# Kernel tuning notes

Hardware: AMD Instinct MI355X
Metric: run time of the kernel (lower is better)

The kernel has to match this reference:

```python
import jax, jax.numpy as jnp
import numpy as np

NUM_CLASSES = 1000
FEATURE_DIM = 256
TEMPERATURE = 0.07
EPS = 1e-12  # matches torch F.normalize default eps


def setup_inputs() -> dict:
    key = jax.random.key(0)
    k1, k2, k3, k4 = jax.random.split(key, 4)
    N = 200000
    return {
        "src_feats": jax.random.normal(k1, (N, FEATURE_DIM), dtype=jnp.float32),
        "src_labels": jax.random.randint(k2, (N,), 0, NUM_CLASSES, dtype=jnp.int64),
        "tgt_feats": jax.random.normal(k3, (N, FEATURE_DIM), dtype=jnp.float32),
        "tgt_labels": jax.random.randint(k4, (N,), 0, NUM_CLASSES, dtype=jnp.int64),
    }


def _l2_normalize(x):
    norm = jnp.sqrt(jnp.sum(x * x, axis=1, keepdims=True))
    return x / jnp.maximum(norm, EPS)


def _prototype_init(features, labels):
    """Single-pass segment-mean replacing the per-class python loop.
    prototypes[c] = mean of features with label==c (0 if class absent)."""
    sums = jax.ops.segment_sum(features, labels, num_segments=NUM_CLASSES)  # [C, D]
    counts = jax.ops.segment_sum(jnp.ones_like(labels, dtype=features.dtype),
                                 labels, num_segments=NUM_CLASSES)          # [C]
    protos = sums / jnp.maximum(counts, 1.0)[:, None]
    return protos, counts


def _structure_matrix(protos):
    p = _l2_normalize(protos)
    return p @ p.T  # [C, C]


def reference(src_feats, src_labels, tgt_feats, tgt_labels):
    # PrototypeBank.update with detached features (first call: plain segment-mean)
    src_protos, _ = _prototype_init(jax.lax.stop_gradient(src_feats), src_labels)
    tgt_protos, _ = _prototype_init(jax.lax.stop_gradient(tgt_feats), tgt_labels)

    src_struct = _structure_matrix(src_protos)
    tgt_struct = _structure_matrix(tgt_protos)
    struct_loss = jnp.mean((src_struct - tgt_struct) ** 2)

    # contrastive loss: cosine logits against source prototypes, cross-entropy
    feats_n = _l2_normalize(src_feats)
    protos_n = _l2_normalize(src_protos)
    logits = (feats_n @ protos_n.T) / TEMPERATURE  # [N, C]
    logp = jax.nn.log_softmax(logits, axis=1)
    contrast_loss = -jnp.mean(jnp.take_along_axis(logp, src_labels[:, None], axis=1))

    return struct_loss, contrast_loss, src_protos, src_struct
```

## Files before the change

kernel.cpp:

```cpp
#include <hip/hip_runtime.h>
#include <hip/hip_fp8.h>

#define NCLS 1000
#define DIM 256
#define GCAP 500
#define NT16 64
#define SCLF 20.609930f
#define CP 23.0f
#define CPLN2 15.94238515f
#define LN2 0.69314718056f
#define PADC 2.86102294921875e-06f

typedef __attribute__((ext_vector_type(4))) float f32x4;
typedef long long i64;
typedef unsigned long long u64;

#if defined(__has_builtin) && __has_builtin(__builtin_amdgcn_cvt_pk_fp8_f32)
#define CVTPK(a, b, old, hi) __builtin_amdgcn_cvt_pk_fp8_f32((a), (b), (old), (hi))
#else
__device__ __forceinline__ unsigned cvtpk_sw(float a, float b, unsigned old, bool hi) {
  unsigned lo8 = __hip_cvt_float_to_fp8(a, __HIP_SATFINITE, __HIP_E4M3);
  unsigned hi8 = __hip_cvt_float_to_fp8(b, __HIP_SATFINITE, __HIP_E4M3);
  unsigned pk = lo8 | (hi8 << 8);
  return hi ? ((old & 0xffffu) | (pk << 16)) : ((old & 0xffff0000u) | pk);
}
#define CVTPK(a, b, old, hi) cvtpk_sw((a), (b), (old), (hi))
#endif

__device__ __forceinline__ float fexp2(float x) {
#if __has_builtin(__builtin_amdgcn_exp2f)
  return __builtin_amdgcn_exp2f(x);
#else
  return exp2f(x);
#endif
}

__global__ __launch_bounds__(256) void scatter_kernel(
    const int* __restrict__ sl, const int* __restrict__ tl, int N,
    int* __restrict__ gcnt, int* __restrict__ glist) {
  const int i = blockIdx.x * 256 + threadIdx.x;
  if (i >= 2 * N) return;
  const int side = (i >= N) ? 1 : 0;
  const int r = i - side * N;
  const int c = (side ? tl : sl)[r];
  const int bin = side * NCLS + c;
  const int slot = atomicAdd(gcnt + bin, 1);
  if (slot < GCAP) glist[(size_t)bin * GCAP + slot] = r;
}

__global__ __launch_bounds__(256) void proto_kernel(
    const float* __restrict__ sf, const float* __restrict__ tf,
    const int* __restrict__ gcnt, const int* __restrict__ glist,
    float* __restrict__ mean_out, float* __restrict__ spn, float* __restrict__ tpn,
    unsigned char* __restrict__ pbf8) {
  const int bid = blockIdx.x;
  const int side = (bid < NCLS) ? 1 : 0;
  const int c = side ? bid : (bid - NCLS);
  const int bin = side * NCLS + c;
  const float* feats = side ? tf : sf;
  const int* list = glist + (size_t)bin * GCAP;
  const int m = min(gcnt[bin], GCAP);
  const int t = threadIdx.x;
  __shared__ float s_red[4];

  float a0 = 0.f, a1 = 0.f, a2 = 0.f, a3 = 0.f, a4 = 0.f, a5 = 0.f, a6 = 0.f, a7 = 0.f;
  int i = 0;
  for (; i + 8 <= m; i += 8) {
    a0 += feats[(size_t)list[i + 0] * DIM + t];
    a1 += feats[(size_t)list[i + 1] * DIM + t];
    a2 += feats[(size_t)list[i + 2] * DIM + t];
    a3 += feats[(size_t)list[i + 3] * DIM + t];
    a4 += feats[(size_t)list[i + 4] * DIM + t];
    a5 += feats[(size_t)list[i + 5] * DIM + t];
    a6 += feats[(size_t)list[i + 6] * DIM + t];
    a7 += feats[(size_t)list[i + 7] * DIM + t];
  }
  for (; i < m; i++) a0 += feats[(size_t)list[i] * DIM + t];
  const float sum = ((a0 + a1) + (a2 + a3)) + ((a4 + a5) + (a6 + a7));
  const float mean = sum / fmaxf((float)m, 1.0f);
  if (!side) mean_out[(size_t)c * DIM + t] = mean;

  float ss = mean * mean;
  #pragma unroll
  for (int o = 1; o < 64; o <<= 1) ss += __shfl_xor(ss, o);
  if ((t & 63) == 0) s_red[t >> 6] = ss;
  __syncthreads();
  const float tot = s_red[0] + s_red[1] + s_red[2] + s_red[3];
  const float innv = 1.0f / fmaxf(sqrtf(tot), 1e-12f);
  const float p = mean * innv;
  (side ? tpn : spn)[(size_t)c * DIM + t] = p;
  if (!side) {
    size_t off = (size_t)(c >> 4) * 4096 + (size_t)(t >> 6) * 1024
               + (size_t)((t >> 3) & 3) * 256 + (size_t)(c & 15) * 16
               + (size_t)((t >> 5) & 1) * 8 + (t & 7);
    unsigned q = CVTPK(p, p, 0u, false);
    pbf8[off] = (unsigned char)(q & 0xffu);
  }
}

__global__ __launch_bounds__(256, 3) void fused_kernel(
    const float* __restrict__ feats, const int* __restrict__ labels,
    const unsigned char* __restrict__ pbf8, float* __restrict__ accp,
    const float* __restrict__ spn, const float* __restrict__ tpn,
    float* __restrict__ out_struct, float* __restrict__ acc,
    int N, int cblocks) {
  __shared__ __align__(16) unsigned char lds_raw[34816];
  const int bid = blockIdx.x;
  const int t = threadIdx.x;

  if (bid < 256) {
    float (*Sa)[68] = (float(*)[68])(lds_raw);
    float (*Sb)[68] = (float(*)[68])(lds_raw + 4352);
    float (*Ta)[68] = (float(*)[68])(lds_raw + 8704);
    float (*Tb)[68] = (float(*)[68])(lds_raw + 13056);
    float* red = (float*)(lds_raw + 17408);
    const int tx = t & 15, ty = t >> 4;
    const int i0 = (bid >> 4) * 64, j0 = (bid & 15) * 64;
    float cs[4][4], cg[4][4];
    #pragma unroll
    for (int a = 0; a < 4; a++)
      #pragma unroll
      for (int b = 0; b < 4; b++) { cs[a][b] = 0.f; cg[a][b] = 0.f; }

    const int srow = t >> 2;
    const int skq = (t & 3) * 4;
    for (int k0 = 0; k0 < DIM; k0 += 16) {
      __syncthreads();
      {
        float4 z = make_float4(0.f, 0.f, 0.f, 0.f);
        int ra = i0 + srow, rb = j0 + srow;
        float4 va = (ra < NCLS) ? *(const float4*)(spn + (size_t)ra * DIM + k0 + skq) : z;
        float4 vb = (rb < NCLS) ? *(const float4*)(spn + (size_t)rb * DIM + k0 + skq) : z;
        float4 wa = (ra < NCLS) ? *(const float4*)(tpn + (size_t)ra * DIM + k0 + skq) : z;
        float4 wb = (rb < NCLS) ? *(const float4*)(tpn + (size_t)rb * DIM + k0 + skq) : z;
        Sa[skq+0][srow]=va.x; Sa[skq+1][srow]=va.y; Sa[skq+2][srow]=va.z; Sa[skq+3][srow]=va.w;
        Sb[skq+0][srow]=vb.x; Sb[skq+1][srow]=vb.y; Sb[skq+2][srow]=vb.z; Sb[skq+3][srow]=vb.w;
        Ta[skq+0][srow]=wa.x; Ta[skq+1][srow]=wa.y; Ta[skq+2][srow]=wa.z; Ta[skq+3][srow]=wa.w;
        Tb[skq+0][srow]=wb.x; Tb[skq+1][srow]=wb.y; Tb[skq+2][srow]=wb.z; Tb[skq+3][srow]=wb.w;
      }
      __syncthreads();
      #pragma unroll
      for (int k = 0; k < 16; k++) {
        float a[4], b[4], c[4], d[4];
        *(float4*)a = *(const float4*)&Sa[k][ty * 4];
        *(float4*)b = *(const float4*)&Sb[k][tx * 4];
        *(float4*)c = *(const float4*)&Ta[k][ty * 4];
        *(float4*)d = *(const float4*)&Tb[k][tx * 4];
        #pragma unroll
        for (int ii = 0; ii < 4; ii++)
          #pragma unroll
          for (int jj = 0; jj < 4; jj++) {
            cs[ii][jj] = fmaf(a[ii], b[jj], cs[ii][jj]);
            cg[ii][jj] = fmaf(c[ii], d[jj], cg[ii][jj]);
          }
      }
    }
    float d2 = 0.f;
    #pragma unroll
    for (int ii = 0; ii < 4; ii++) {
      int gi = i0 + ty * 4 + ii;
      if (gi < NCLS) {
        #pragma unroll
        for (int jj = 0; jj < 4; jj++) {
          int gj = j0 + tx * 4 + jj;
          if (gj < NCLS) {
            out_struct[(size_t)gi * NCLS + gj] = cs[ii][jj];
            float df = cs[ii][jj] - cg[ii][jj];
            d2 += df * df;
          }
        }
      }
    }
    red[t] = d2;
    __syncthreads();
    for (int o = 128; o > 0; o >>= 1) { if (t < o) red[t] += red[t + o]; __syncthreads(); }
    if (t == 0) atomicAdd(acc, red[0]);
    return;
  }

  const int cbid = bid - 256;
  if (cbid >= cblocks) return;
  const int lane = t & 63;
  const int w = t >> 6;
  const int lx = lane & 15, lg = lane >> 4;
  const int row0 = cbid * 128 + w * 32;
  const float4 z4 = make_float4(0.f, 0.f, 0.f, 0.f);
  const unsigned char* bbase = pbf8 + (lg << 8) + (lx << 4);
  float* Aw = (float*)lds_raw + (size_t)w * (32 * 68);

  i64 af[2][8];
  float sclF[2][4];
  float sSt[2][4];
  int lbR[2];

  float n2a[2] = {0.f, 0.f};
  for (int kc = 0; kc < 4; kc++) {
    #pragma unroll
    for (int i = 0; i < 8; i++) {
      const int f = i * 64 + lane;
      const int row = f >> 4;
      const int c4 = f & 15;
      const int gr = row0 + row;
      float4 v = (gr < N) ? *(const float4*)(feats + (size_t)gr * DIM + kc * 64 + c4 * 4) : z4;
      *(float4*)&Aw[row * 68 + c4 * 4] = v;
    }
    #pragma unroll
    for (int rf = 0; rf < 2; rf++) {
      const int row = rf * 16 + lx;
      #pragma unroll
      for (int kk = 0; kk < 2; kk++) {
        float4 x = *(const float4*)&Aw[row * 68 + kk * 32 + lg * 8];
        float4 y = *(const float4*)&Aw[row * 68 + kk * 32 + lg * 8 + 4];
        n2a[rf] += x.x*x.x + x.y*x.y + x.z*x.z + x.w*x.w
                 + y.x*y.x + y.y*y.y + y.z*y.z + y.w*y.w;
        unsigned w0 = CVTPK(x.x, x.y, 0u, false);
        w0 = CVTPK(x.z, x.w, w0, true);
        unsigned w1 = CVTPK(y.x, y.y, 0u, false);
        w1 = CVTPK(y.z, y.w, w1, true);
        af[rf][kc * 2 + kk] = (i64)(((u64)w1 << 32) | (u64)w0);
      }
    }
  }
  #pragma unroll
  for (int rf = 0; rf < 2; rf++) {
    const int r = row0 + rf * 16 + lx;
    lbR[rf] = (r < N) ? labels[r] : 0;
    float n2 = n2a[rf];
    n2 += __shfl_xor(n2, 16);
    n2 += __shfl_xor(n2, 32);
    const float sw = SCLF / fmaxf(sqrtf(n2), 1e-12f);
    #pragma unroll
    for (int reg = 0; reg < 4; reg++) {
      sclF[rf][reg] = __shfl(sw, (lg << 2) | reg);
      sSt[rf][reg] = 0.f;
    }
  }

  int4 bA[4], bB[4];

  #define LOADB(dst_, cf_)                                                      \
    {                                                                           \
      const int4* gp = (const int4*)(bbase + ((size_t)(cf_) << 12));            \
      _Pragma("unroll")                                                         \
      for (int q = 0; q < 4; q++) dst_[q] = gp[q << 6];                         \
    }

  #define COMPUTE(buf_)                                                         \
    {                                                                           \
      f32x4 d0 = {0.f, 0.f, 0.f, 0.f};                                          \
      f32x4 d1 = {0.f, 0.f, 0.f, 0.f};                                          \
      _Pragma("unroll")                                                         \
      for (int q = 0; q < 4; q++) {                                             \
        i64 e0 = ((const i64*)&buf_[q])[0];                                     \
        i64 e1 = ((const i64*)&buf_[q])[1];                                     \
        d0 = __builtin_amdgcn_mfma_f32_16x16x32_fp8_fp8(af[0][2*q],   e0, d0, 0, 0, 0); \
        d1 = __builtin_amdgcn_mfma_f32_16x16x32_fp8_fp8(af[1][2*q],   e0, d1, 0, 0, 0); \
        d0 = __builtin_amdgcn_mfma_f32_16x16x32_fp8_fp8(af[0][2*q+1], e1, d0, 0, 0, 0); \
        d1 = __builtin_amdgcn_mfma_f32_16x16x32_fp8_fp8(af[1][2*q+1], e1, d1, 0, 0, 0); \
      }                                                                         \
      _Pragma("unroll")                                                         \
      for (int reg = 0; reg < 4; reg++) {                                       \
        sSt[0][reg] += fexp2(fmaf(d0[reg], sclF[0][reg], -CP));                 \
        sSt[1][reg] += fexp2(fmaf(d1[reg], sclF[1][reg], -CP));                 \
      }                                                                         \
    }

  LOADB(bA, 0);
  for (int cf = 0; cf < NT16; cf += 2) {
    LOADB(bB, cf + 1);
    COMPUTE(bA);
    if (cf + 2 < NT16) LOADB(bA, cf + 2);
    COMPUTE(bB);
  }

  float dvalS[2];
  #pragma unroll
  for (int rf = 0; rf < 2; rf++) {
    const int lb = lbR[rf];
    const unsigned char* gB = pbf8 + ((size_t)(lb >> 4) << 12) + (lg << 8)
                            + ((size_t)(lb & 15) << 4);
    f32x4 dL = {0.f, 0.f, 0.f, 0.f};
    #pragma unroll
    for (int q = 0; q < 4; q++) {
      int4 bg = *(const int4*)(gB + (q << 10));
      i64 e0 = ((const i64*)&bg)[0];
      i64 e1 = ((const i64*)&bg)[1];
      dL = __builtin_amdgcn_mfma_f32_16x16x32_fp8_fp8(af[rf][2*q],   e0, dL, 0, 0, 0);
      dL = __builtin_amdgcn_mfma_f32_16x16x32_fp8_fp8(af[rf][2*q+1], e1, dL, 0, 0, 0);
    }
    const int sel = lx & 3;
    dvalS[rf] = (sel == 0) ? dL[0] : (sel == 1) ? dL[1] : (sel == 2) ? dL[2] : dL[3];
  }

  float wl = 0.f;
  #pragma unroll
  for (int rf = 0; rf < 2; rf++)
    #pragma unroll
    for (int reg = 0; reg < 4; reg++) {
      float s = sSt[rf][reg];
      #pragma unroll
      for (int o = 1; o < 16; o <<= 1) s += __shfl_xor(s, o);
      const int j = (lg << 2) + reg;
      const float lbraw = __shfl(dvalS[rf], ((j >> 2) << 4) | j);
      const int row = row0 + rf * 16 + j;
      if (lx == 0 && row < N)
        wl += logf(s - PADC) + CPLN2 - lbraw * sclF[rf][reg] * LN2;
    }

  #pragma unroll
  for (int o = 1; o < 64; o <<= 1) wl += __shfl_xor(wl, o);
  if (lane == 0) atomicAdd(accp + (cbid & 63), wl);
}

__global__ void final_kernel(const float* __restrict__ acc,
                             const float* __restrict__ accp,
                             float* __restrict__ out, int N) {
  float c = 0.f;
  for (int i = 0; i < 64; i++) c += accp[i];
  out[0] = acc[0] * (1.0f / (float)(NCLS * NCLS));
  out[1] = c / (float)N;
}

extern "C" void kernel_launch(void* const* d_in, const int* in_sizes, int n_in,
                              void* d_out, int out_size, void* d_ws, size_t ws_size,
                              hipStream_t stream) {
  const float* src_feats  = (const float*)d_in[0];
  const int*   src_labels = (const int*)d_in[1];
  const float* tgt_feats  = (const float*)d_in[2];
  const int*   tgt_labels = (const int*)d_in[3];
  const int N = in_sizes[0] / DIM;

  float* ws = (float*)d_ws;
  float* acc    = ws;
  float* src_pn = ws + 16;
  float* tgt_pn = ws + 256016;
  unsigned char* pbf8 = (unsigned char*)(ws + 512016);
  int* gcnt = (int*)(ws + 643088);
  float* accp = ws + 645088;

  float* out_f      = (float*)d_out;
  float* out_protos = out_f + 2;
  float* out_struct = out_f + 2 + NCLS * DIM;
  int* glist = (int*)out_struct;

  hipMemsetAsync(acc, 0, 2 * sizeof(float), stream);
  hipMemsetAsync(gcnt, 0, 2 * NCLS * sizeof(int), stream);
  hipMemsetAsync(accp, 0, 64 * sizeof(float), stream);
  hipMemsetAsync(pbf8 + 62 * 4096, 0, 2 * 4096, stream);

  int sblocks = (2 * N + 255) / 256;
  scatter_kernel<<<sblocks, 256, 0, stream>>>(src_labels, tgt_labels, N, gcnt, glist);

  proto_kernel<<<2 * NCLS, 256, 0, stream>>>(src_feats, tgt_feats, gcnt, glist,
                                             out_protos, src_pn, tgt_pn, pbf8);

  int cblocks = (N + 127) / 128;
  fused_kernel<<<256 + cblocks, 256, 0, stream>>>(
      src_feats, src_labels, pbf8, accp, src_pn, tgt_pn, out_struct, acc, N, cblocks);

  final_kernel<<<1, 1, 0, stream>>>(acc, accp, out_f, N);
}
```

Measured before the change: 314.0 us.

## Vectorize prototype gather, shrink fused-kernel LDS staging, merge memsets

The prototype kernel now splits rows of each class across four wavefronts, each doing float4 loads over the full feature row, with partial sums reduced through shared memory. This replaces one-scalar-per-thread gathers with wider, more coalesced loads and more independent rows in flight. The contrastive part of the fused kernel stages features in 32-column chunks instead of 64, nearly halving its LDS footprint, which may allow more resident blocks per CU. The workspace is reordered so that three small memsets collapse into one.

```diff
diff --git a/kernel.cpp b/kernel.cpp
--- a/kernel.cpp
+++ b/kernel.cpp
@@ -61,22 +61,34 @@
   const int* list = glist + (size_t)bin * GCAP;
   const int m = min(gcnt[bin], GCAP);
   const int t = threadIdx.x;
+  const int q = t >> 6, l = t & 63;
+  __shared__ float Sp[4][256];
   __shared__ float s_red[4];
 
-  float a0 = 0.f, a1 = 0.f, a2 = 0.f, a3 = 0.f, a4 = 0.f, a5 = 0.f, a6 = 0.f, a7 = 0.f;
-  int i = 0;
-  for (; i + 8 <= m; i += 8) {
-    a0 += feats[(size_t)list[i + 0] * DIM + t];
-    a1 += feats[(size_t)list[i + 1] * DIM + t];
-    a2 += feats[(size_t)list[i + 2] * DIM + t];
-    a3 += feats[(size_t)list[i + 3] * DIM + t];
-    a4 += feats[(size_t)list[i + 4] * DIM + t];
-    a5 += feats[(size_t)list[i + 5] * DIM + t];
-    a6 += feats[(size_t)list[i + 6] * DIM + t];
-    a7 += feats[(size_t)list[i + 7] * DIM + t];
-  }
-  for (; i < m; i++) a0 += feats[(size_t)list[i] * DIM + t];
-  const float sum = ((a0 + a1) + (a2 + a3)) + ((a4 + a5) + (a6 + a7));
+  float4 A[8];
+  #pragma unroll
+  for (int u = 0; u < 8; u++) A[u] = make_float4(0.f, 0.f, 0.f, 0.f);
+  int i = q;
+  for (; i + 28 < m; i += 32) {
+    #pragma unroll
+    for (int u = 0; u < 8; u++) {
+      const float4 v = *(const float4*)(feats + (size_t)list[i + 4 * u] * DIM + l * 4);
+      A[u].x += v.x; A[u].y += v.y; A[u].z += v.z; A[u].w += v.w;
+    }
+  }
+  for (; i < m; i += 4) {
+    const float4 v = *(const float4*)(feats + (size_t)list[i] * DIM + l * 4);
+    A[0].x += v.x; A[0].y += v.y; A[0].z += v.z; A[0].w += v.w;
+  }
+  float4 s4;
+  s4.x = ((A[0].x + A[1].x) + (A[2].x + A[3].x)) + ((A[4].x + A[5].x) + (A[6].x + A[7].x));
+  s4.y = ((A[0].y + A[1].y) + (A[2].y + A[3].y)) + ((A[4].y + A[5].y) + (A[6].y + A[7].y));
+  s4.z = ((A[0].z + A[1].z) + (A[2].z + A[3].z)) + ((A[4].z + A[5].z) + (A[6].z + A[7].z));
+  s4.w = ((A[0].w + A[1].w) + (A[2].w + A[3].w)) + ((A[4].w + A[5].w) + (A[6].w + A[7].w));
+  *(float4*)&Sp[q][l * 4] = s4;
+  __syncthreads();
+
+  const float sum = ((Sp[0][t] + Sp[1][t]) + (Sp[2][t] + Sp[3][t]));
   const float mean = sum / fmaxf((float)m, 1.0f);
   if (!side) mean_out[(size_t)c * DIM + t] = mean;
 
@@ -93,8 +105,8 @@
     size_t off = (size_t)(c >> 4) * 4096 + (size_t)(t >> 6) * 1024
                + (size_t)((t >> 3) & 3) * 256 + (size_t)(c & 15) * 16
                + (size_t)((t >> 5) & 1) * 8 + (t & 7);
-    unsigned q = CVTPK(p, p, 0u, false);
-    pbf8[off] = (unsigned char)(q & 0xffu);
+    unsigned qq = CVTPK(p, p, 0u, false);
+    pbf8[off] = (unsigned char)(qq & 0xffu);
   }
 }
 
@@ -104,7 +116,7 @@
     const float* __restrict__ spn, const float* __restrict__ tpn,
     float* __restrict__ out_struct, float* __restrict__ acc,
     int N, int cblocks) {
-  __shared__ __align__(16) unsigned char lds_raw[34816];
+  __shared__ __align__(16) unsigned char lds_raw[18432];
   const int bid = blockIdx.x;
   const int t = threadIdx.x;
 
@@ -186,7 +198,7 @@
   const int row0 = cbid * 128 + w * 32;
   const float4 z4 = make_float4(0.f, 0.f, 0.f, 0.f);
   const unsigned char* bbase = pbf8 + (lg << 8) + (lx << 4);
-  float* Aw = (float*)lds_raw + (size_t)w * (32 * 68);
+  float* Aw = (float*)lds_raw + (size_t)w * (32 * 36);
 
   i64 af[2][8];
   float sclF[2][4];
@@ -194,31 +206,28 @@
   int lbR[2];
 
   float n2a[2] = {0.f, 0.f};
-  for (int kc = 0; kc < 4; kc++) {
-    #pragma unroll
-    for (int i = 0; i < 8; i++) {
+  for (int kc = 0; kc < 8; kc++) {
+    #pragma unroll
+    for (int i = 0; i < 4; i++) {
       const int f = i * 64 + lane;
-      const int row = f >> 4;
-      const int c4 = f & 15;
+      const int row = f >> 3;
+      const int c4 = f & 7;
       const int gr = row0 + row;
-      float4 v = (gr < N) ? *(const float4*)(feats + (size_t)gr * DIM + kc * 64 + c4 * 4) : z4;
-      *(float4*)&Aw[row * 68 + c4 * 4] = v;
+      float4 v = (gr < N) ? *(const float4*)(feats + (size_t)gr * DIM + kc * 32 + c4 * 4) : z4;
+      *(float4*)&Aw[row * 36 + c4 * 4] = v;
     }
     #pragma unroll
     for (int rf = 0; rf < 2; rf++) {
       const int row = rf * 16 + lx;
-      #pragma unroll
-      for (int kk = 0; kk < 2; kk++) {
-        float4 x = *(const float4*)&Aw[row * 68 + kk * 32 + lg * 8];
-        float4 y = *(const float4*)&Aw[row * 68 + kk * 32 + lg * 8 + 4];
-        n2a[rf] += x.x*x.x + x.y*x.y + x.z*x.z + x.w*x.w
-                 + y.x*y.x + y.y*y.y + y.z*y.z + y.w*y.w;
-        unsigned w0 = CVTPK(x.x, x.y, 0u, false);
-        w0 = CVTPK(x.z, x.w, w0, true);
-        unsigned w1 = CVTPK(y.x, y.y, 0u, false);
-        w1 = CVTPK(y.z, y.w, w1, true);
-        af[rf][kc * 2 + kk] = (i64)(((u64)w1 << 32) | (u64)w0);
-      }
+      float4 x = *(const float4*)&Aw[row * 36 + lg * 8];
+      float4 y = *(const float4*)&Aw[row * 36 + lg * 8 + 4];
+      n2a[rf] += x.x*x.x + x.y*x.y + x.z*x.z + x.w*x.w
+               + y.x*y.x + y.y*y.y + y.z*y.z + y.w*y.w;
+      unsigned w0 = CVTPK(x.x, x.y, 0u, false);
+      w0 = CVTPK(x.z, x.w, w0, true);
+      unsigned w1 = CVTPK(y.x, y.y, 0u, false);
+      w1 = CVTPK(y.z, y.w, w1, true);
+      af[rf][kc] = (i64)(((u64)w1 << 32) | (u64)w0);
     }
   }
   #pragma unroll
@@ -332,20 +341,18 @@
 
   float* ws = (float*)d_ws;
   float* acc    = ws;
-  float* src_pn = ws + 16;
-  float* tgt_pn = ws + 256016;
-  unsigned char* pbf8 = (unsigned char*)(ws + 512016);
-  int* gcnt = (int*)(ws + 643088);
-  float* accp = ws + 645088;
+  int*   gcnt   = (int*)(ws + 16);
+  float* accp   = ws + 2016;
+  float* src_pn = ws + 2080;
+  float* tgt_pn = ws + 258080;
+  unsigned char* pbf8 = (unsigned char*)(ws + 514080);
 
   float* out_f      = (float*)d_out;
   float* out_protos = out_f + 2;
   float* out_struct = out_f + 2 + NCLS * DIM;
   int* glist = (int*)out_struct;
 
-  hipMemsetAsync(acc, 0, 2 * sizeof(float), stream);
-  hipMemsetAsync(gcnt, 0, 2 * NCLS * sizeof(int), stream);
-  hipMemsetAsync(accp, 0, 64 * sizeof(float), stream);
+  hipMemsetAsync(ws, 0, 2080 * sizeof(float), stream);
   hipMemsetAsync(pbf8 + 62 * 4096, 0, 2 * 4096, stream);
 
   int sblocks = (2 * N + 255) / 256;
```

Result: no change. 318.1 us (+1.3%).
